# Kernel optimization log

Measured on AMD Instinct MI355X. Metric: run time of the kernel, lower is better.

The kernel has to match this reference:

```python
import jax, jax.numpy as jnp
import numpy as np

N, IN, HID, OUT, HD = 512, 256, 256, 256, 64  # n_agents, in_dim, hid_dim, out_dim, head_dim (out_dim // n_heads)


def _mlp2(x, w1, b1, w2, b2):
    return jax.nn.relu(x @ w1.T + b1) @ w2.T + b2


def setup_inputs():
    key = jax.random.key(0)
    ks = jax.random.split(key, 32)
    p = lambda i, shape: jax.random.normal(ks[i], shape, dtype=jnp.float32) * 0.05
    V = jax.random.normal(ks[0], (N, IN), dtype=jnp.float32)
    adj = jax.random.randint(ks[1], (N, N), 0, 2, dtype=jnp.int32)
    adj = adj.at[jnp.arange(N), jnp.arange(N)].set(1)  # self-loops so no softmax row is all -inf
    prev_hidden = jax.random.normal(ks[2], (N, HID), dtype=jnp.float32)
    return {
        "V": V, "adj": adj, "prev_hidden": prev_hidden,
        "W1": p(3, (HID, IN)), "sa0": p(4, (HID,)), "sa1": p(5, (HID,)),
        "ce_w1": p(6, (HID, 2 * IN)), "ce_b1": p(7, (HID,)), "ce_w2": p(8, (HD, HID)), "ce_b2": p(9, (HD,)),
        "ca0": p(10, (HD,)), "ca1": p(11, (HD,)),
        "te_w1": p(12, (HID, IN + HID)), "te_b1": p(13, (HID,)), "te_w2": p(14, (HD, HID)), "te_b2": p(15, (HD,)),
        "ta0": p(16, (HD,)), "ta1": p(17, (HD,)),
        "pe_w1": p(18, (HID, 3 * IN)), "pe_b1": p(19, (HID,)), "pe_w2": p(20, (HD, HID)), "pe_b2": p(21, (HD,)),
        "pa0": p(22, (HD,)), "pa1": p(23, (HD,)),
        "W2": p(24, (OUT, HID + 2 * HD + 1)), "op_w": p(25, (OUT, OUT)), "op_b": p(26, (OUT,)),
        "ln_g": jnp.ones((OUT,), jnp.float32), "ln_b": jnp.zeros((OUT,), jnp.float32),
    }


def _forward(V, adj, prev_hidden, W1, sa0, sa1, ce_w1, ce_b1, ce_w2, ce_b2, ca0, ca1,
             te_w1, te_b1, te_w2, te_b2, ta0, ta1, pe_w1, pe_b1, pe_w2, pe_b2, pa0, pa1,
             W2, op_w, op_b, ln_g, ln_b):
    neg = -jnp.inf
    # --- branch 1: standard GAT attention ---
    Wh1 = V @ W1.T                                             # (N, HID)
    s1 = (Wh1 @ sa0)[:, None] + (Wh1 @ sa1)[None, :]           # (N, N)
    s1 = jnp.where(adj == 0, neg, s1)
    H1 = jax.nn.softmax(s1, axis=1) @ Wh1                      # (N, HID)
    # --- branch 2: causal, all ordered pairs i != j ---
    wA, wB = ce_w1[:, :IN], ce_w1[:, IN:]
    h = jax.nn.relu((V @ wA.T)[:, None, :] + (V @ wB.T)[None, :, :] + ce_b1)  # (N, N, HID)
    f = h @ ce_w2.T + ce_b2                                    # (N, N, HD)
    s2 = jnp.where(jnp.eye(N, dtype=bool), neg, f @ (ca0 + ca1))
    a2 = jax.nn.softmax(s2.reshape(-1)).reshape(N, N)          # softmax over all off-diagonal pairs
    H2 = jnp.broadcast_to(jnp.einsum('ij,ijd->d', a2, f), (N, HD))
    # --- branch 3: temporal; (N,1) scores broadcast against (N,N) causal mask ---
    tf = _mlp2(jnp.concatenate([V, prev_hidden], -1), te_w1, te_b1, te_w2, te_b2)  # (N, HD)
    ts = tf @ (ta0 + ta1)                                      # (N,)
    cmask = jnp.triu(jnp.ones((N, N), dtype=bool), 1)
    s3 = jnp.where(cmask, neg, jnp.broadcast_to(ts[:, None], (N, N)))
    H3 = jax.nn.softmax(s3, axis=1) @ tf                       # (N, HD) == prefix means of tf
    # --- branch 4: cooperative; first two neighbors in index order (zeros if < 2) ---
    pos = jnp.where(adj == 1, jnp.arange(N)[None, :], N)
    srt = jnp.sort(pos, axis=1)
    i0, i1 = srt[:, 0], srt[:, 1]
    valid = (i1 < N)[:, None]
    n0 = jnp.where(valid, V[jnp.clip(i0, 0, N - 1)], 0.0)
    n1 = jnp.where(valid, V[jnp.clip(i1, 0, N - 1)], 0.0)
    cf = _mlp2(jnp.concatenate([V, n0, n1], -1), pe_w1, pe_b1, pe_w2, pe_b2)  # (N, HD)
    # torch: softmax over dim of size 1 -> all ones, alpha^T @ cf == column sums -> (HD,)
    # then unsqueezed to (HD,1) and zero-padded to (N,1) since HD < N  (faithful to source bug)
    H4v = cf.sum(axis=0)
    H4 = jnp.concatenate([H4v, jnp.zeros((N - HD,), V.dtype)])[:, None]       # (N, 1)
    # --- combine ---
    Hc = jnp.concatenate([H1, H2, H3, H4], axis=-1) @ W2.T     # (N, OUT)
    out = Hc @ op_w.T + op_b
    mu = out.mean(-1, keepdims=True)
    var = ((out - mu) ** 2).mean(-1, keepdims=True)
    y = (out - mu) / jnp.sqrt(var + 1e-5) * ln_g + ln_b        # LayerNorm, eps=1e-5
    return jax.nn.elu(y)                                       # dropout is identity in eval


def reference(V, adj, prev_hidden, W1, sa0, sa1, ce_w1, ce_b1, ce_w2, ce_b2, ca0, ca1,
              te_w1, te_b1, te_w2, te_b2, ta0, ta1, pe_w1, pe_b1, pe_w2, pe_b2, pa0, pa1,
              W2, op_w, op_b, ln_g, ln_b):
    return _forward(V, adj, prev_hidden, W1, sa0, sa1, ce_w1, ce_b1, ce_w2, ce_b2, ca0, ca1,
                    te_w1, te_b1, te_w2, te_b2, ta0, ta1, pe_w1, pe_b1, pe_w2, pe_b2, pa0, pa1,
                    W2, op_w, op_b, ln_g, ln_b)
```

## Files before the change

### kernel.cpp

```cpp
#include <hip/hip_runtime.h>

typedef unsigned short u16;

constexpr int kN   = 512;
constexpr int kIN  = 256;
constexpr int kHID = 256;
constexpr int kHD  = 64;
constexpr int kOUT = 256;

__device__ __forceinline__ float us2f(u16 u){
  union { unsigned int i; float f; } c; c.i = ((unsigned int)u) << 16; return c.f;
}
__device__ __forceinline__ u16 f2us(float f){
  union { float f; unsigned int i; } c; c.f = f;
  unsigned int r = c.i + 0x7fff + ((c.i >> 16) & 1);
  return (u16)(r >> 16);
}
__device__ __forceinline__ float ldraw(const void* p, size_t i, bool f32){
  return f32 ? ((const float*)p)[i] : us2f(((const u16*)p)[i]);
}

__device__ bool probe_is_f32(const unsigned int* __restrict__ V){
  __shared__ int cnt;
  if (threadIdx.x == 0) cnt = 0;
  __syncthreads();
  int c = 0;
  for (int k = threadIdx.x; k < 4096; k += 256){
    float x = us2f((u16)(V[k] & 0xffffu));
    if (!(fabsf(x) <= 32.0f)) c++;
  }
  atomicAdd(&cnt, c);
  __syncthreads();
  return cnt > 64;
}

__device__ __forceinline__ float blk_red(float v, float* tmp, bool isMax){
  int lane = threadIdx.x & 63, wv = threadIdx.x >> 6;
  #pragma unroll
  for (int o = 32; o > 0; o >>= 1){
    float t = __shfl_down(v, o, 64);
    v = isMax ? fmaxf(v, t) : (v + t);
  }
  __syncthreads();
  if (lane == 0) tmp[wv] = v;
  __syncthreads();
  float r = tmp[0];
  for (int i = 1; i < 4; ++i) r = isMax ? fmaxf(r, tmp[i]) : (r + tmp[i]);
  return r;
}

constexpr int kNConv = 23;
struct ConvArgs { const void* src[kNConv]; float* dst[kNConv]; int n[kNConv]; };
struct GSeg2 { const float* X; const float* W; float* C; int ldx, ldw, ldc, K; };
struct GS32 { const float* X; const float* W; float* C; int ldx, ldw, ldc, K; int bkn; };

struct Args {
  const unsigned int* Vraw;
  const int* adj;
  int* flag; void* out;
  const void *rca0,*rca1,*rcw2,*rcb2,*rtw2,*rpw2;
  float *Vf,*prevf,*W1f,*sa1f,*cw1f,*cb1f,*cw2f,*cb2f,*ca0f,*ca1f;
  float *tw1f,*tb1f,*tw2f,*tb2f,*pw1f,*pb1f,*pw2f,*pb2f;
  float *W2f,*opwf,*opbf,*lngf,*lnbf;
  float *tw2t,*pw2t,*Wcomb,*OM,*ow4;
  float *Wh1,*e1v,*wadj,*Hc,*Am,*Bm,*uvec,*beta;
  float *s2,*maxp,*zp,*MZ,*gsum;
  float *htp0,*htp1,*hpp0,*hpp1,*hpp2,*hidden_t,*hidden_p;
  float *tfm,*cfm,*H4v,*Xp,*out3;
  ConvArgs ca;
  GSeg2 gs[8];
};

__device__ __forceinline__ void gemm32_body(const GS32 sg, int tm, int tn, int tid,
                                            float* Xs, float* Ws)
{
  const int i0 = tm << 5, n0 = tn << 5;
  const int xrow = tid >> 3;
  const int xk = (tid & 7) << 2;
  const int rg = (tid >> 4) << 1;
  const int cg = (tid & 15) << 1;
  const float* Xb = sg.X + (size_t)i0 * sg.ldx;
  const float* Wb = sg.bkn ? (sg.W + n0) : (sg.W + (size_t)n0 * sg.ldw);
  float4 xr, wr;
  auto loadT = [&](int kt){
    xr = *(const float4*)(Xb + (size_t)xrow * sg.ldx + kt + xk);
    if (sg.bkn) wr = *(const float4*)(Wb + (size_t)(kt + xrow) * sg.ldw + xk);
    else        wr = *(const float4*)(Wb + (size_t)xrow * sg.ldw + kt + xk);
  };
  auto writeT = [&](int bu){
    float* xs = Xs + bu*1152;
    xs[(xk+0)*36 + xrow] = xr.x; xs[(xk+1)*36 + xrow] = xr.y;
    xs[(xk+2)*36 + xrow] = xr.z; xs[(xk+3)*36 + xrow] = xr.w;
    float* wsp = Ws + bu*1152;
    if (sg.bkn){
      wsp[xrow*36 + xk+0] = wr.x; wsp[xrow*36 + xk+1] = wr.y;
      wsp[xrow*36 + xk+2] = wr.z; wsp[xrow*36 + xk+3] = wr.w;
    } else {
      wsp[(xk+0)*36 + xrow] = wr.x; wsp[(xk+1)*36 + xrow] = wr.y;
      wsp[(xk+2)*36 + xrow] = wr.z; wsp[(xk+3)*36 + xrow] = wr.w;
    }
  };
  loadT(0); writeT(0); __syncthreads();
  float a00=0,a01=0,a10=0,a11=0;
  const int nkt = sg.K >> 5;
  for (int t = 0; t < nkt; ++t){
    if (t+1 < nkt) loadT((t+1) << 5);
    const float* xs = Xs + (t&1)*1152;
    const float* wsp = Ws + (t&1)*1152;
    #pragma unroll
    for (int kk = 0; kk < 32; ++kk){
      float2 av = *(const float2*)&xs[kk*36 + rg];
      float2 bv = *(const float2*)&wsp[kk*36 + cg];
      a00 += av.x*bv.x; a01 += av.x*bv.y;
      a10 += av.y*bv.x; a11 += av.y*bv.y;
    }
    if (t+1 < nkt) writeT((t+1)&1);
    __syncthreads();
  }
  float* cp = sg.C + (size_t)(i0+rg)*sg.ldc + n0 + cg;
  *(float2*)cp = make_float2(a00, a01);
  *(float2*)(cp + sg.ldc) = make_float2(a10, a11);
}

__device__ void body_gemmA(const Args& A, int it, int tid, char* SM)
{
  float (*Xs)[32][68] = (float (*)[32][68])SM;
  float (*Ws)[32][68] = (float (*)[32][68])(SM + 17408);
  int seg = it >> 5, x = it & 31;
  const GSeg2 sg = A.gs[seg];
  const int tm = x & 7, tn = x >> 3;
  const int i0 = tm << 6, n0 = tn << 6;

  const int xrow = tid >> 3;
  const int xk   = (tid & 7) << 2;
  const int rg = (tid >> 4) << 2;
  const int cg = (tid & 15) << 2;

  const float* Xb = sg.X + (size_t)i0 * sg.ldx;
  const float* Wb = sg.W + (size_t)n0 * sg.ldw;

  float4 xr0, xr1, wr0, wr1;
  auto loadT = [&](int kt){
    xr0 = *(const float4*)(Xb + (size_t)xrow * sg.ldx + kt + xk);
    xr1 = *(const float4*)(Xb + (size_t)(xrow+32) * sg.ldx + kt + xk);
    wr0 = *(const float4*)(Wb + (size_t)xrow * sg.ldw + kt + xk);
    wr1 = *(const float4*)(Wb + (size_t)(xrow+32) * sg.ldw + kt + xk);
  };
  auto writeT = [&](int bu){
    Xs[bu][xk+0][xrow] = xr0.x;  Xs[bu][xk+1][xrow] = xr0.y;
    Xs[bu][xk+2][xrow] = xr0.z;  Xs[bu][xk+3][xrow] = xr0.w;
    Xs[bu][xk+0][xrow+32] = xr1.x;  Xs[bu][xk+1][xrow+32] = xr1.y;
    Xs[bu][xk+2][xrow+32] = xr1.z;  Xs[bu][xk+3][xrow+32] = xr1.w;
    Ws[bu][xk+0][xrow]    = wr0.x; Ws[bu][xk+1][xrow]    = wr0.y;
    Ws[bu][xk+2][xrow]    = wr0.z; Ws[bu][xk+3][xrow]    = wr0.w;
    Ws[bu][xk+0][xrow+32] = wr1.x; Ws[bu][xk+1][xrow+32] = wr1.y;
    Ws[bu][xk+2][xrow+32] = wr1.z; Ws[bu][xk+3][xrow+32] = wr1.w;
  };

  loadT(0); writeT(0); __syncthreads();

  float acc[4][4] = {};
  const int nkt = sg.K >> 5;
  for (int t = 0; t < nkt; ++t){
    if (t + 1 < nkt) loadT((t + 1) << 5);
    const int bu = t & 1;
    #pragma unroll
    for (int kk = 0; kk < 32; ++kk){
      const float4 av = *(const float4*)&Xs[bu][kk][rg];
      const float4 bv = *(const float4*)&Ws[bu][kk][cg];
      acc[0][0]+=av.x*bv.x; acc[0][1]+=av.x*bv.y; acc[0][2]+=av.x*bv.z; acc[0][3]+=av.x*bv.w;
      acc[1][0]+=av.y*bv.x; acc[1][1]+=av.y*bv.y; acc[1][2]+=av.y*bv.z; acc[1][3]+=av.y*bv.w;
      acc[2][0]+=av.z*bv.x; acc[2][1]+=av.z*bv.y; acc[2][2]+=av.z*bv.z; acc[2][3]+=av.z*bv.w;
      acc[3][0]+=av.w*bv.x; acc[3][1]+=av.w*bv.y; acc[3][2]+=av.w*bv.z; acc[3][3]+=av.w*bv.w;
    }
    if (t + 1 < nkt) writeT((t + 1) & 1);
    __syncthreads();
  }

  #pragma unroll
  for (int ri = 0; ri < 4; ++ri)
    *(float4*)(sg.C + (size_t)(i0 + rg + ri) * sg.ldc + (n0 + cg)) =
      make_float4(acc[ri][0], acc[ri][1], acc[ri][2], acc[ri][3]);

  if (seg == 0){
    int cb = n0 + cg;
    float s0 = A.sa1f[cb], s1 = A.sa1f[cb+1], s2v = A.sa1f[cb+2], s3 = A.sa1f[cb+3];
    #pragma unroll
    for (int ri = 0; ri < 4; ++ri){
      float v = acc[ri][0]*s0 + acc[ri][1]*s1 + acc[ri][2]*s2v + acc[ri][3]*s3;
      v += __shfl_xor(v, 1, 16);
      v += __shfl_xor(v, 2, 16);
      v += __shfl_xor(v, 4, 16);
      v += __shfl_xor(v, 8, 16);
      if ((tid & 15) == 0) atomicAdd(&A.e1v[i0 + rg + ri], v);
    }
  }
}

__global__ __launch_bounds__(256) void k_s0(Args A)
{
  __shared__ __align__(16) char SM[16896];
  int it = blockIdx.x, tid = threadIdx.x;
  bool f32 = probe_is_f32(A.Vraw);
  if (it < 256){
    if (it == 0){
      if (tid == 0) *A.flag = f32 ? 1 : 0;
      A.e1v[tid] = 0.f; A.e1v[tid + 256] = 0.f;
    }
    int t = it*256 + tid;
    for (int s = 0; s < kNConv; ++s){
      int n4 = A.ca.n[s] >> 2;
      float4* d = (float4*)A.ca.dst[s];
      if (f32){
        const float4* sf = (const float4*)A.ca.src[s];
        for (int i = t; i < n4; i += 65536) d[i] = sf[i];
      } else {
        const ushort4* sb = (const ushort4*)A.ca.src[s];
        for (int i = t; i < n4; i += 65536){
          ushort4 u = sb[i];
          d[i] = make_float4(us2f(u.x), us2f(u.y), us2f(u.z), us2f(u.w));
        }
      }
    }
  } else if (it < 768){
    unsigned long long* msk = (unsigned long long*)SM;
    int* sj = (int*)(SM + 64);
    int i = it - 256;
    int w = tid >> 6, lane = tid & 63;
    unsigned long long m0 = __ballot(A.adj[(size_t)i*kN + tid] != 0);
    unsigned long long m1 = __ballot(A.adj[(size_t)i*kN + 256 + tid] != 0);
    if (lane == 0){ msk[w] = m0; msk[4 + w] = m1; }
    __syncthreads();
    if (tid == 0){
      int j0 = -1, j1 = -1;
      for (int c = 0; c < 8 && j1 < 0; ++c){
        unsigned long long m = msk[c];
        while (m && j1 < 0){
          int bb = __builtin_ctzll(m);
          int j = c*64 + bb;
          if (j0 < 0) j0 = j; else j1 = j;
          m &= m - 1;
        }
      }
      if (j1 < 0) j0 = -1;
      sj[0] = j0; sj[1] = j1;
    }
    __syncthreads();
    int j0 = sj[0], j1 = sj[1];
    A.Xp[(size_t)i*768 + tid]       = ldraw(A.Vraw, (size_t)i*kIN + tid, f32);
    A.Xp[(size_t)i*768 + 256 + tid] = (j0 >= 0) ? ldraw(A.Vraw, (size_t)j0*kIN + tid, f32) : 0.f;
    A.Xp[(size_t)i*768 + 512 + tid] = (j1 >= 0) ? ldraw(A.Vraw, (size_t)j1*kIN + tid, f32) : 0.f;
  } else if (it == 768){
    float* st = (float*)SM;
    if (tid < 64){ st[tid] = ldraw(A.rca0, tid, f32) + ldraw(A.rca1, tid, f32); A.H4v[tid] = 0.f; }
    __syncthreads();
    float a = 0.f;
    for (int d = 0; d < kHD; ++d) a += ldraw(A.rcw2, (size_t)d*kHID + tid, f32) * st[d];
    A.uvec[tid] = a;
    if (tid == 0){
      float b = 0.f;
      for (int d = 0; d < kHD; ++d) b += ldraw(A.rcb2, d, f32) * st[d];
      *A.beta = b;
    }
  } else {
    const void* src = (it == 769) ? A.rtw2 : A.rpw2;
    float* dst = (it == 769) ? A.tw2t : A.pw2t;
    float* st = (float*)SM;
    for (int ch = 0; ch < 4; ++ch){
      __syncthreads();
      #pragma unroll
      for (int e = 0; e < 16; ++e){
        int lin = e*256 + tid, r = lin >> 6, c = lin & 63;
        st[r*65 + c] = ldraw(src, (size_t)r*256 + ch*64 + c, f32);
      }
      __syncthreads();
      #pragma unroll
      for (int e = 0; e < 16; ++e){
        int lin = e*256 + tid, kc = lin >> 6, dd = lin & 63;
        dst[(size_t)(ch*64 + kc)*64 + dd] = st[dd*65 + kc];
      }
    }
  }
}

__global__ __launch_bounds__(256) void k_s1(Args A)
{
  __shared__ __align__(16) char SM[34816];
  int it = blockIdx.x, tid = threadIdx.x;
  if (it < 256){
    body_gemmA(A, it, tid, SM);
  } else if (it < 336){
    int q = it - 256, tm = q & 7, tn = q >> 3;
    const float* Wsrc = A.W2f + ((tn < 8) ? 0 : 64);
    GS32 sg{A.opwf, Wsrc, A.Wcomb, 256, 385, 320, 256, 1};
    gemm32_body(sg, tm, tn, tid, (float*)SM, (float*)(SM + 9216));
  } else if (it < 352){
    int q = it - 336;
    GS32 sg{A.opwf, A.W2f + 256, A.OM, 256, 385, 64, 256, 1};
    gemm32_body(sg, q & 7, q >> 3, tid, (float*)SM, (float*)(SM + 9216));
  } else {
    float* st = (float*)SM;
    st[tid] = A.W2f[(size_t)tid*385 + 384];
    __syncthreads();
    float a = 0.f;
    const float* orow = A.opwf + (size_t)tid*256;
    for (int m = 0; m < 256; m += 4){
      float4 o4 = *(const float4*)(orow + m);
      a += o4.x*st[m] + o4.y*st[m+1] + o4.z*st[m+2] + o4.w*st[m+3];
    }
    A.ow4[tid] = a;
  }
}

__global__ __launch_bounds__(256) void k_s2(Args A)
{
  __shared__ float SM2[8];
  int it = blockIdx.x, tid = threadIdx.x;
  if (it < 128){
    int f = it*256 + tid;
    int c4 = f & 63;
    {
      float4 a = ((const float4*)A.htp0)[f], bb = ((const float4*)A.htp1)[f];
      float4 bi = ((const float4*)A.tb1f)[c4];
      ((float4*)A.hidden_t)[f] = make_float4(
        fmaxf(a.x+bb.x+bi.x,0.f), fmaxf(a.y+bb.y+bi.y,0.f),
        fmaxf(a.z+bb.z+bi.z,0.f), fmaxf(a.w+bb.w+bi.w,0.f));
    }
    {
      float4 a = ((const float4*)A.hpp0)[f], bb = ((const float4*)A.hpp1)[f];
      float4 c = ((const float4*)A.hpp2)[f];
      float4 bi = ((const float4*)A.pb1f)[c4];
      ((float4*)A.hidden_p)[f] = make_float4(
        fmaxf(a.x+bb.x+c.x+bi.x,0.f), fmaxf(a.y+bb.y+c.y+bi.y,0.f),
        fmaxf(a.z+bb.z+c.z+bi.z,0.f), fmaxf(a.w+bb.w+c.w+bi.w,0.f));
    }
  } else {
    int i = it - 128;
    int m0 = A.adj[(size_t)i*kN + tid];
    int m1 = A.adj[(size_t)i*kN + tid + 256];
    float ea = A.e1v[tid], eb = A.e1v[tid+256];
    float v0 = m0 ? ea : -1e30f;
    float v1 = m1 ? eb : -1e30f;
    float m = blk_red(fmaxf(v0, v1), SM2, true);
    float z = blk_red((m0 ? expf(ea-m) : 0.f) + (m1 ? expf(eb-m) : 0.f), SM2, false);
    float iz = 1.0f / z;
    A.wadj[(size_t)i*kN + tid]       = m0 ? expf(ea - m) * iz : 0.f;
    A.wadj[(size_t)i*kN + tid + 256] = m1 ? expf(eb - m) * iz : 0.f;
  }
}

__global__ __launch_bounds__(256) void k_s3(Args A)
{
  __shared__ __align__(16) float SM3[4*256 + 256];
  int it = blockIdx.x, tid = threadIdx.x;
  if (it < 64){
    int m = it >> 5, grp = it & 31;
    const float* X  = m ? A.hidden_p : A.hidden_t;
    const float* Wt = m ? A.pw2t : A.tw2t;
    const float* bi = m ? A.pb2f : A.tb2f;
    float* C = m ? A.cfm : A.tfm;
    int i0 = grp*16 + (tid >> 6)*4;
    int d = tid & 63;
    const float* x0 = X + (size_t)i0*256;
    const float* x1 = x0 + 256;
    const float* x2 = x0 + 512;
    const float* x3 = x0 + 768;
    float a0=0.f, a1=0.f, a2=0.f, a3=0.f;
    for (int k = 0; k < 256; k += 4){
      float w0 = Wt[(size_t)(k+0)*64 + d];
      float w1 = Wt[(size_t)(k+1)*64 + d];
      float w2 = Wt[(size_t)(k+2)*64 + d];
      float w3 = Wt[(size_t)(k+3)*64 + d];
      float4 f0 = *(const float4*)(x0 + k);
      float4 f1 = *(const float4*)(x1 + k);
      float4 f2 = *(const float4*)(x2 + k);
      float4 f3 = *(const float4*)(x3 + k);
      a0 += f0.x*w0 + f0.y*w1 + f0.z*w2 + f0.w*w3;
      a1 += f1.x*w0 + f1.y*w1 + f1.z*w2 + f1.w*w3;
      a2 += f2.x*w0 + f2.y*w1 + f2.z*w2 + f2.w*w3;
      a3 += f3.x*w0 + f3.y*w1 + f3.z*w2 + f3.w*w3;
    }
    float bd = bi[d];
    C[(size_t)(i0+0)*64 + d] = a0 + bd;
    C[(size_t)(i0+1)*64 + d] = a1 + bd;
    C[(size_t)(i0+2)*64 + d] = a2 + bd;
    C[(size_t)(i0+3)*64 + d] = a3 + bd;
  } else {
    float* aib = SM3;
    float* uu  = SM3 + 1024;
    int q = it - 64;
    int i0 = (q & 127) * 4, jt = q >> 7;
    int w = tid >> 6, lane = tid & 63;
    uu[tid] = A.uvec[tid];
    float b1v = A.cb1f[tid];
    #pragma unroll
    for (int r = 0; r < 4; ++r) aib[r*256 + tid] = A.Am[(size_t)(i0+r)*kHID + tid] + b1v;
    __syncthreads();
    float bet = *A.beta;
    float4 u4 = *(const float4*)&uu[lane*4];
    float4 a4[4];
    #pragma unroll
    for (int r = 0; r < 4; ++r) a4[r] = *(const float4*)&aib[r*256 + lane*4];
    float sv[4] = {-1e30f, -1e30f, -1e30f, -1e30f};
    int jbase = jt*128 + w*32;
    for (int jj = 0; jj < 32; ++jj){
      int j = jbase + jj;
      float4 bv = *(const float4*)(A.Bm + (size_t)j*kHID + lane*4);
      #pragma unroll
      for (int r = 0; r < 4; ++r){
        float p = fmaxf(a4[r].x+bv.x,0.f)*u4.x + fmaxf(a4[r].y+bv.y,0.f)*u4.y
                + fmaxf(a4[r].z+bv.z,0.f)*u4.z + fmaxf(a4[r].w+bv.w,0.f)*u4.w;
        #pragma unroll
        for (int o = 32; o > 0; o >>= 1) p += __shfl_xor(p, o, 64);
        p += bet;
        if (j == i0 + r) p = -1e30f;
        if (lane == jj) sv[r] = p;
      }
    }
    float lmax = -1e30f;
    if (lane < 32){
      #pragma unroll
      for (int r = 0; r < 4; ++r){
        A.s2[(size_t)(i0+r)*kN + jbase + lane] = sv[r];
        lmax = fmaxf(lmax, sv[r]);
      }
    }
    float m = lmax;
    #pragma unroll
    for (int o = 32; o > 0; o >>= 1) m = fmaxf(m, __shfl_xor(m, o, 64));
    float z = 0.f;
    if (lane < 32){
      #pragma unroll
      for (int r = 0; r < 4; ++r) z += expf(sv[r] - m);
    }
    #pragma unroll
    for (int o = 32; o > 0; o >>= 1) z += __shfl_xor(z, o, 64);
    if (lane == 0){
      int pb = q*4 + w;
      A.maxp[pb] = m; A.zp[pb] = z;
    }
  }
}

__global__ __launch_bounds__(256) void k_s4(Args A)
{
  __shared__ __align__(16) char SM[18432];
  int it = blockIdx.x, tid = threadIdx.x;
  if (it < 128){
    GS32 sg{A.wadj, A.Wh1, A.Hc, 512, 256, 320, 512, 1};
    gemm32_body(sg, it & 15, it >> 4, tid, (float*)SM, (float*)(SM + 9216));
  } else if (it < 192){
    int d = it - 128;
    int lane = tid & 63, wv = tid >> 6;
    float v0 = A.tfm[(size_t)(2*tid)*kHD + d];
    float v1 = A.tfm[(size_t)(2*tid+1)*kHD + d];
    float s = v0 + v1;
    float x = s;
    #pragma unroll
    for (int off = 1; off < 64; off <<= 1){
      float y = __shfl_up(x, off, 64);
      if (lane >= off) x += y;
    }
    float* wsum = (float*)SM;
    if (lane == 63) wsum[wv] = x;
    __syncthreads();
    float base = 0.f;
    for (int k = 0; k < wv; ++k) base += wsum[k];
    float excl = base + x - s;
    A.Hc[(size_t)(2*tid)*320 + 256 + d]   = (excl + v0) / (float)(2*tid + 1);
    A.Hc[(size_t)(2*tid+1)*320 + 256 + d] = (excl + s)  / (float)(2*tid + 2);
  } else if (it < 200){
    float* sm = (float*)SM;
    int d = tid & 63, sub = tid >> 6;
    int r0 = (it-192)*64 + sub*16;
    float s = 0.f;
    #pragma unroll
    for (int e = 0; e < 16; ++e) s += A.cfm[(size_t)(r0+e)*kHD + d];
    sm[sub*64 + d] = s;
    __syncthreads();
    if (tid < 64)
      atomicAdd(&A.H4v[tid], sm[tid] + sm[64+tid] + sm[128+tid] + sm[192+tid]);
  } else {
    float* red = (float*)SM;
    float m = -1e30f;
    #pragma unroll
    for (int r = 0; r < 8; ++r) m = fmaxf(m, A.maxp[tid + 256*r]);
    m = blk_red(m, red, true);
    float z = 0.f;
    #pragma unroll
    for (int r = 0; r < 8; ++r) z += A.zp[tid + 256*r] * expf(A.maxp[tid + 256*r] - m);
    z = blk_red(z, red, false);
    if (tid == 0){ A.MZ[0] = m; A.MZ[1] = z; }
    A.gsum[tid] = 0.f;
  }
}

__global__ __launch_bounds__(256) void k_s5(Args A)
{
  __shared__ __align__(16) char SM[18432];
  int it = blockIdx.x, tid = threadIdx.x;
  if (it < 1024){
    float* wt = (float*)SM;
    int i0 = (it & 31) * 16, j0 = (it >> 5) * 16;
    float M = A.MZ[0], invZ = 1.0f / A.MZ[1];
    {
      int r = tid >> 4, c = tid & 15;
      wt[r*16 + c] = expf(A.s2[(size_t)(i0+r)*kN + (j0+c)] - M) * invZ;
    }
    float b1v = A.cb1f[tid];
    float aib[16];
    #pragma unroll
    for (int r = 0; r < 16; ++r) aib[r] = A.Am[(size_t)(i0+r)*kHID + tid] + b1v;
    __syncthreads();
    float acc = 0.f;
    for (int j = 0; j < 16; ++j){
      float bj = A.Bm[(size_t)(j0+j)*kHID + tid];
      #pragma unroll
      for (int r = 0; r < 16; ++r)
        acc += wt[r*16 + j] * fmaxf(aib[r] + bj, 0.f);
    }
    atomicAdd(&A.gsum[tid], acc);
  } else {
    int q = it - 1024;
    GS32 sg{A.Hc, A.Wcomb, A.out3, 320, 320, 256, 320, 0};
    gemm32_body(sg, q & 15, q >> 4, tid, (float*)SM, (float*)(SM + 9216));
  }
}

__global__ __launch_bounds__(256) void k_s6(Args A)
{
  __shared__ float gs[kHID];
  __shared__ float part[kHD][4];
  __shared__ float h2s[kHD];
  __shared__ float cc2s[kOUT];
  int b = blockIdx.x, tid = threadIdx.x;
  bool f32 = (*A.flag != 0);
  gs[tid] = A.gsum[tid];
  __syncthreads();
  {
    int dd = tid >> 2, q = tid & 3;
    float a = 0.f;
    for (int kk = 0; kk < 64; ++kk){
      int k = q*64 + kk;
      a += gs[k] * A.cw2f[(size_t)dd*kHID + k];
    }
    part[dd][q] = a;
  }
  __syncthreads();
  if (tid < kHD)
    h2s[tid] = A.cb2f[tid] + part[tid][0] + part[tid][1] + part[tid][2] + part[tid][3];
  __syncthreads();
  {
    float a = 0.f;
    const float* om = A.OM + (size_t)tid*64;
    for (int d = 0; d < kHD; d += 4){
      float4 o4 = *(const float4*)(om + d);
      a += o4.x*h2s[d] + o4.y*h2s[d+1] + o4.z*h2s[d+2] + o4.w*h2s[d+3];
    }
    cc2s[tid] = a;
  }
  __syncthreads();
  int row = b*4 + (tid >> 6), lane = tid & 63;
  float h4r = (row < kHD) ? A.H4v[row] : 0.f;
  float4 v  = *(const float4*)(A.out3 + (size_t)row*kOUT + lane*4);
  float4 c2 = *(const float4*)(&cc2s[lane*4]);
  float4 o4 = *(const float4*)(A.ow4 + lane*4);
  float4 pb = *(const float4*)(A.opbf + lane*4);
  v.x += c2.x + h4r*o4.x + pb.x;
  v.y += c2.y + h4r*o4.y + pb.y;
  v.z += c2.z + h4r*o4.z + pb.z;
  v.w += c2.w + h4r*o4.w + pb.w;
  float s = v.x + v.y + v.z + v.w;
  #pragma unroll
  for (int o = 32; o > 0; o >>= 1) s += __shfl_xor(s, o, 64);
  float mu = s * (1.0f/kOUT);
  float dx = v.x-mu, dy = v.y-mu, dz = v.z-mu, dw = v.w-mu;
  float ss = dx*dx + dy*dy + dz*dz + dw*dw;
  #pragma unroll
  for (int o = 32; o > 0; o >>= 1) ss += __shfl_xor(ss, o, 64);
  float rs = rsqrtf(ss * (1.0f/kOUT) + 1e-5f);
  float4 g  = *(const float4*)(A.lngf + lane*4);
  float4 be = *(const float4*)(A.lnbf + lane*4);
  float y0 = dx*rs*g.x + be.x, y1 = dy*rs*g.y + be.y;
  float y2 = dz*rs*g.z + be.z, y3 = dw*rs*g.w + be.w;
  y0 = (y0 > 0.f) ? y0 : expm1f(y0);
  y1 = (y1 > 0.f) ? y1 : expm1f(y1);
  y2 = (y2 > 0.f) ? y2 : expm1f(y2);
  y3 = (y3 > 0.f) ? y3 : expm1f(y3);
  if (f32){
    *(float4*)((float*)A.out + (size_t)row*kOUT + lane*4) = make_float4(y0,y1,y2,y3);
  } else {
    ushort4 u; u.x = f2us(y0); u.y = f2us(y1); u.z = f2us(y2); u.w = f2us(y3);
    ((ushort4*)A.out)[(size_t)row*64 + lane] = u;
  }
}

extern "C" void kernel_launch(void* const* d_in, const int* in_sizes, int n_in,
                              void* d_out, int out_size, void* d_ws, size_t ws_size,
                              hipStream_t stream)
{
  const void* V     = d_in[0];
  const int*  adj   = (const int*)d_in[1];
  const void* prev  = d_in[2];
  const void* W1    = d_in[3];
  const void* sa1   = d_in[5];
  const void* ce_w1 = d_in[6];
  const void* ce_b1 = d_in[7];
  const void* ce_w2 = d_in[8];
  const void* ce_b2 = d_in[9];
  const void* ca0   = d_in[10];
  const void* ca1   = d_in[11];
  const void* te_w1 = d_in[12];
  const void* te_b1 = d_in[13];
  const void* te_w2 = d_in[14];
  const void* te_b2 = d_in[15];
  const void* pe_w1 = d_in[18];
  const void* pe_b1 = d_in[19];
  const void* pe_w2 = d_in[20];
  const void* pe_b2 = d_in[21];
  const void* W2    = d_in[24];
  const void* op_w  = d_in[25];
  const void* op_b  = d_in[26];
  const void* ln_g  = d_in[27];
  const void* ln_b  = d_in[28];

  float* ws  = (float*)d_ws;
  int*  flag = (int*)ws;
  float* p   = ws + 16;
  float* Vf   = p; p += 131072;
  float* prevf= p; p += 131072;
  float* W1f  = p; p += 65536;
  float* sa1f = p; p += 256;
  float* cw1f = p; p += 131072;
  float* cb1f = p; p += 256;
  float* cw2f = p; p += 16384;
  float* cb2f = p; p += 64;
  float* ca0f = p; p += 64;
  float* ca1f = p; p += 64;
  float* tw1f = p; p += 131072;
  float* tb1f = p; p += 256;
  float* tw2f = p; p += 16384;
  float* tb2f = p; p += 64;
  float* pw1f = p; p += 196608;
  float* pb1f = p; p += 256;
  float* pw2f = p; p += 16384;
  float* pb2f = p; p += 64;
  float* W2f  = p; p += 98560;
  float* opwf = p; p += 65536;
  float* opbf = p; p += 256;
  float* lngf = p; p += 256;
  float* lnbf = p; p += 256;
  float* tw2t = p; p += 16384;
  float* pw2t = p; p += 16384;
  float* Wcomb= p; p += 81920;
  float* OM   = p; p += 16384;
  float* ow4  = p; p += 256;
  float* Wh1      = p; p += 131072;
  float* e1v      = p; p += 512;
  float* wadj     = p; p += 262144;
  float* Hc       = p; p += 163840;
  float* Am       = p; p += 131072;
  float* Bm       = p; p += 131072;
  float* uvec     = p; p += 256;
  float* beta     = p; p += 16;
  float* s2       = p; p += 262144;
  float* maxp     = p; p += 4096;
  float* zpart    = p; p += 4096;
  float* MZ       = p; p += 16;
  float* gsum     = p; p += 256;
  float* htp0     = p; p += 131072;
  float* htp1     = p; p += 131072;
  float* hpp0     = p; p += 131072;
  float* hpp1     = p; p += 131072;
  float* hpp2     = p; p += 131072;
  float* hidden_t = p; p += 131072;
  float* hidden_p = p; p += 131072;
  float* tfm      = p; p += 32768;
  float* cfm      = p; p += 32768;
  float* H4v      = p; p += 64;
  float* Xp       = p; p += 393216;
  float* out3     = p; p += 131072;

  Args A;
  A.Vraw = (const unsigned int*)V; A.adj = adj;
  A.flag = flag; A.out = d_out;
  A.rca0 = ca0; A.rca1 = ca1; A.rcw2 = ce_w2; A.rcb2 = ce_b2; A.rtw2 = te_w2; A.rpw2 = pe_w2;
  A.Vf=Vf; A.prevf=prevf; A.W1f=W1f; A.sa1f=sa1f; A.cw1f=cw1f; A.cb1f=cb1f;
  A.cw2f=cw2f; A.cb2f=cb2f; A.ca0f=ca0f; A.ca1f=ca1f;
  A.tw1f=tw1f; A.tb1f=tb1f; A.tw2f=tw2f; A.tb2f=tb2f;
  A.pw1f=pw1f; A.pb1f=pb1f; A.pw2f=pw2f; A.pb2f=pb2f;
  A.W2f=W2f; A.opwf=opwf; A.opbf=opbf; A.lngf=lngf; A.lnbf=lnbf;
  A.tw2t=tw2t; A.pw2t=pw2t; A.Wcomb=Wcomb; A.OM=OM; A.ow4=ow4;
  A.Wh1=Wh1; A.e1v=e1v; A.wadj=wadj; A.Hc=Hc;
  A.Am=Am; A.Bm=Bm; A.uvec=uvec; A.beta=beta;
  A.s2=s2; A.maxp=maxp; A.zp=zpart; A.MZ=MZ; A.gsum=gsum;
  A.htp0=htp0; A.htp1=htp1; A.hpp0=hpp0; A.hpp1=hpp1; A.hpp2=hpp2;
  A.hidden_t=hidden_t; A.hidden_p=hidden_p;
  A.tfm=tfm; A.cfm=cfm; A.H4v=H4v; A.Xp=Xp; A.out3=out3;

  {
    const void* srcs[kNConv] = {V, prev, W1, sa1, ce_w1, ce_b1, ce_w2, ce_b2, ca0, ca1,
                                te_w1, te_b1, te_w2, te_b2, pe_w1, pe_b1, pe_w2, pe_b2,
                                W2, op_w, op_b, ln_g, ln_b};
    float* dsts[kNConv] = {Vf, prevf, W1f, sa1f, cw1f, cb1f, cw2f, cb2f, ca0f, ca1f,
                           tw1f, tb1f, tw2f, tb2f, pw1f, pb1f, pw2f, pb2f,
                           W2f, opwf, opbf, lngf, lnbf};
    int ns[kNConv] = {131072, 131072, 65536, 256, 131072, 256, 16384, 64, 64, 64,
                      131072, 256, 16384, 64, 196608, 256, 16384, 64,
                      98560, 65536, 256, 256, 256};
    for (int s = 0; s < kNConv; ++s){ A.ca.src[s] = srcs[s]; A.ca.dst[s] = dsts[s]; A.ca.n[s] = ns[s]; }
  }
  A.gs[0] = {Vf,       W1f,        Wh1,  256, 256, 256, 256};
  A.gs[1] = {Vf,       cw1f,       Am,   256, 512, 256, 256};
  A.gs[2] = {Vf,       cw1f + 256, Bm,   256, 512, 256, 256};
  A.gs[3] = {Vf,       tw1f,       htp0, 256, 512, 256, 256};
  A.gs[4] = {prevf,    tw1f + 256, htp1, 256, 512, 256, 256};
  A.gs[5] = {Xp,       pw1f,       hpp0, 768, 768, 256, 256};
  A.gs[6] = {Xp + 256, pw1f + 256, hpp1, 768, 768, 256, 256};
  A.gs[7] = {Xp + 512, pw1f + 512, hpp2, 768, 768, 256, 256};

  k_s0<<<771,  256, 0, stream>>>(A);
  k_s1<<<353,  256, 0, stream>>>(A);
  k_s2<<<640,  256, 0, stream>>>(A);
  k_s3<<<576,  256, 0, stream>>>(A);
  k_s4<<<201,  256, 0, stream>>>(A);
  k_s5<<<1152, 256, 0, stream>>>(A);
  k_s6<<<128,  256, 0, stream>>>(A);
}
```

Baseline: 254.6 us.

## Tile pairwise causal score computation as 32x32 register-blocked shared-memory tiles

Replaces the per-row-group scoring loop, which did one 64-lane shuffle reduction per (i,j) pair, with a 32x32 output tile per block. Each block stages A+b1 and B slices transposed in shared memory and accumulates a 2x2 register block per thread over k. This removes the shuffle-reduction overhead and reuses the loaded A/B data across many pairs. Partial max/sum outputs drop from 2048 to 256 per block-level reduction, and the launch is resized to match.

```diff
diff --git a/kernel.cpp b/kernel.cpp
--- a/kernel.cpp
+++ b/kernel.cpp
@@ -351,7 +351,7 @@
 
 __global__ __launch_bounds__(256) void k_s3(Args A)
 {
-  __shared__ __align__(16) float SM3[4*256 + 256];
+  __shared__ __align__(16) float SM3[32*36*2 + 256 + 256 + 8];
   int it = blockIdx.x, tid = threadIdx.x;
   if (it < 64){
     int m = it >> 5, grp = it & 31;
@@ -386,59 +386,62 @@
     C[(size_t)(i0+2)*64 + d] = a2 + bd;
     C[(size_t)(i0+3)*64 + d] = a3 + bd;
   } else {
-    float* aib = SM3;
-    float* uu  = SM3 + 1024;
+    float* As = SM3;
+    float* Bs = As + 32*36;
+    float* Us = Bs + 32*36;
+    float* B1 = Us + 256;
+    float* red = B1 + 256;
     int q = it - 64;
-    int i0 = (q & 127) * 4, jt = q >> 7;
-    int w = tid >> 6, lane = tid & 63;
-    uu[tid] = A.uvec[tid];
-    float b1v = A.cb1f[tid];
+    int i0 = (q & 15) * 32, j0 = (q >> 4) * 32;
+    Us[tid] = A.uvec[tid];
+    B1[tid] = A.cb1f[tid];
+    const int xrow = tid >> 3;
+    const int xk   = (tid & 7) << 2;
+    const int rg = (tid >> 4) << 1;
+    const int cg = (tid & 15) << 1;
+    float acc[2][2] = {};
+    for (int kt = 0; kt < 256; kt += 32){
+      __syncthreads();
+      float4 av = *(const float4*)(A.Am + (size_t)(i0+xrow)*kHID + kt + xk);
+      float4 bv = *(const float4*)(A.Bm + (size_t)(j0+xrow)*kHID + kt + xk);
+      As[(xk+0)*36 + xrow] = av.x + B1[kt+xk+0];
+      As[(xk+1)*36 + xrow] = av.y + B1[kt+xk+1];
+      As[(xk+2)*36 + xrow] = av.z + B1[kt+xk+2];
+      As[(xk+3)*36 + xrow] = av.w + B1[kt+xk+3];
+      Bs[(xk+0)*36 + xrow] = bv.x;
+      Bs[(xk+1)*36 + xrow] = bv.y;
+      Bs[(xk+2)*36 + xrow] = bv.z;
+      Bs[(xk+3)*36 + xrow] = bv.w;
+      __syncthreads();
+      #pragma unroll
+      for (int kk = 0; kk < 32; ++kk){
+        float uk = Us[kt + kk];
+        float2 a2 = *(const float2*)&As[kk*36 + rg];
+        float2 b2 = *(const float2*)&Bs[kk*36 + cg];
+        acc[0][0] += fmaxf(a2.x + b2.x, 0.f) * uk;
+        acc[0][1] += fmaxf(a2.x + b2.y, 0.f) * uk;
+        acc[1][0] += fmaxf(a2.y + b2.x, 0.f) * uk;
+        acc[1][1] += fmaxf(a2.y + b2.y, 0.f) * uk;
+      }
+    }
+    float bet = *A.beta;
+    float sv[2][2];
     #pragma unroll
-    for (int r = 0; r < 4; ++r) aib[r*256 + tid] = A.Am[(size_t)(i0+r)*kHID + tid] + b1v;
-    __syncthreads();
-    float bet = *A.beta;
-    float4 u4 = *(const float4*)&uu[lane*4];
-    float4 a4[4];
-    #pragma unroll
-    for (int r = 0; r < 4; ++r) a4[r] = *(const float4*)&aib[r*256 + lane*4];
-    float sv[4] = {-1e30f, -1e30f, -1e30f, -1e30f};
-    int jbase = jt*128 + w*32;
-    for (int jj = 0; jj < 32; ++jj){
-      int j = jbase + jj;
-      float4 bv = *(const float4*)(A.Bm + (size_t)j*kHID + lane*4);
+    for (int r = 0; r < 2; ++r){
       #pragma unroll
-      for (int r = 0; r < 4; ++r){
-        float p = fmaxf(a4[r].x+bv.x,0.f)*u4.x + fmaxf(a4[r].y+bv.y,0.f)*u4.y
-                + fmaxf(a4[r].z+bv.z,0.f)*u4.z + fmaxf(a4[r].w+bv.w,0.f)*u4.w;
-        #pragma unroll
-        for (int o = 32; o > 0; o >>= 1) p += __shfl_xor(p, o, 64);
-        p += bet;
-        if (j == i0 + r) p = -1e30f;
-        if (lane == jj) sv[r] = p;
+      for (int c = 0; c < 2; ++c){
+        float vsc = acc[r][c] + bet;
+        int i = i0 + rg + r, j = j0 + cg + c;
+        if (i == j) vsc = -1e30f;
+        sv[r][c] = vsc;
+        A.s2[(size_t)i*kN + j] = vsc;
       }
     }
-    float lmax = -1e30f;
-    if (lane < 32){
-      #pragma unroll
-      for (int r = 0; r < 4; ++r){
-        A.s2[(size_t)(i0+r)*kN + jbase + lane] = sv[r];
-        lmax = fmaxf(lmax, sv[r]);
-      }
-    }
-    float m = lmax;
-    #pragma unroll
-    for (int o = 32; o > 0; o >>= 1) m = fmaxf(m, __shfl_xor(m, o, 64));
-    float z = 0.f;
-    if (lane < 32){
-      #pragma unroll
-      for (int r = 0; r < 4; ++r) z += expf(sv[r] - m);
-    }
-    #pragma unroll
-    for (int o = 32; o > 0; o >>= 1) z += __shfl_xor(z, o, 64);
-    if (lane == 0){
-      int pb = q*4 + w;
-      A.maxp[pb] = m; A.zp[pb] = z;
-    }
+    __syncthreads();
+    float m = blk_red(fmaxf(fmaxf(sv[0][0], sv[0][1]), fmaxf(sv[1][0], sv[1][1])), red, true);
+    float z = expf(sv[0][0]-m) + expf(sv[0][1]-m) + expf(sv[1][0]-m) + expf(sv[1][1]-m);
+    z = blk_red(z, red, false);
+    if (tid == 0){ A.maxp[q] = m; A.zp[q] = z; }
   }
 }
 
@@ -482,13 +485,8 @@
       atomicAdd(&A.H4v[tid], sm[tid] + sm[64+tid] + sm[128+tid] + sm[192+tid]);
   } else {
     float* red = (float*)SM;
-    float m = -1e30f;
-    #pragma unroll
-    for (int r = 0; r < 8; ++r) m = fmaxf(m, A.maxp[tid + 256*r]);
-    m = blk_red(m, red, true);
-    float z = 0.f;
-    #pragma unroll
-    for (int r = 0; r < 8; ++r) z += A.zp[tid + 256*r] * expf(A.maxp[tid + 256*r] - m);
+    float m = blk_red(A.maxp[tid], red, true);
+    float z = A.zp[tid] * expf(A.maxp[tid] - m);
     z = blk_red(z, red, false);
     if (tid == 0){ A.MZ[0] = m; A.MZ[1] = z; }
     A.gsum[tid] = 0.f;
@@ -722,7 +720,7 @@
   k_s0<<<771,  256, 0, stream>>>(A);
   k_s1<<<353,  256, 0, stream>>>(A);
   k_s2<<<640,  256, 0, stream>>>(A);
-  k_s3<<<576,  256, 0, stream>>>(A);
+  k_s3<<<320,  256, 0, stream>>>(A);
   k_s4<<<201,  256, 0, stream>>>(A);
   k_s5<<<1152, 256, 0, stream>>>(A);
   k_s6<<<128,  256, 0, stream>>>(A);
```

Result: faster. 235.5 us (-7.5%).
